# Optimization experiments

Hardware: AMD Instinct MI355X
Metric: run time of the kernel (lower is better)

The kernel has to match this reference:

```python
import jax, jax.numpy as jnp
import numpy as np

N = 25000      # n_nodes
K = 16         # k_sparse (out-degree per node)
E = N * K      # n_edges
D = 12         # depth
U = 48         # units
FEATS = 2
EF = 1
EPS = 1e-5     # BatchNorm eps


def _lin(h, W, b):
    return h @ W.T + b


def _bn(h, g, b):
    # training-mode BatchNorm over dim 0 (biased variance, like torch)
    m = h.mean(0)
    v = jnp.mean((h - m) ** 2, axis=0)
    return (h - m) * jax.lax.rsqrt(v + EPS) * g + b


def setup_inputs():
    key = jax.random.key(0)
    ks = iter(jax.random.split(key, 64))

    def nrm(shape, fan):
        return jax.random.normal(next(ks), shape, dtype=jnp.float32) * float(1.0 / np.sqrt(fan))

    inp = {}
    inp['x'] = jax.random.uniform(next(ks), (N, FEATS), dtype=jnp.float32)
    inp['edge_attr'] = jax.random.uniform(next(ks), (E, EF), dtype=jnp.float32)
    src = jnp.repeat(jnp.arange(N, dtype=jnp.int32), K)            # each node has K out-edges
    dst = jax.random.randint(next(ks), (E,), 0, N, dtype=jnp.int32)
    inp['edge_index'] = jnp.stack([src, dst])                       # [2, E]
    inp['v_lin0_W'] = nrm((U, FEATS), FEATS); inp['v_lin0_b'] = nrm((U,), FEATS)
    for nm in ['vW1', 'vW2', 'vW3', 'vW4']:
        inp[nm] = nrm((D, U, U), U)
    for nm in ['vb1', 'vb2', 'vb3', 'vb4']:
        inp[nm] = nrm((D, U), U)
    inp['vbn_g'] = jnp.ones((D, U), jnp.float32); inp['vbn_b'] = jnp.zeros((D, U), jnp.float32)
    inp['e_lin0_W'] = nrm((U, EF), EF); inp['e_lin0_b'] = nrm((U,), EF)
    inp['eW'] = nrm((D, U, U), U); inp['eb'] = nrm((D, U), U)
    inp['ebn_g'] = jnp.ones((D, U), jnp.float32); inp['ebn_b'] = jnp.zeros((D, U), jnp.float32)
    inp['pW0'] = nrm((U, U), U); inp['pb0'] = nrm((U,), U)
    inp['pW1'] = nrm((U, U), U); inp['pb1'] = nrm((U,), U)
    inp['pW2'] = nrm((1, U), U); inp['pb2'] = nrm((1,), U)
    inp['zW0'] = nrm((U, U), U); inp['zb0'] = nrm((U,), U)
    inp['zW1'] = nrm((1, U), U); inp['zb1'] = nrm((1,), U)
    inp['k_sparse'] = K
    return inp


def _forward(edge_index, k_sparse, x, edge_attr, v_lin0_W, v_lin0_b, vW1, vb1, vW2, vb2, vW3, vb3, vW4, vb4, vbn_g, vbn_b, e_lin0_W, e_lin0_b, eW, eb, ebn_g, ebn_b, pW0, pb0, pW1, pb1, pW2, pb2, zW0, zb0, zW1, zb1):
    n = x.shape[0]
    src, dst = edge_index[0], edge_index[1]
    deg = jnp.maximum(jax.ops.segment_sum(jnp.ones((src.shape[0],), x.dtype), src, num_segments=n), 1.0)
    h = jax.nn.silu(_lin(x, v_lin0_W, v_lin0_b))          # [N, U]
    w = jax.nn.silu(_lin(edge_attr, e_lin0_W, e_lin0_b))  # [E, U]

    def layer(carry, p):
        h, w = carry
        W1, b1, W2, b2, W3, b3, W4, b4, gv, bv, We, be, ge, bee = p
        h1 = _lin(h, W1, b1); h2 = _lin(h, W2, b2)
        h3 = _lin(h, W3, b3); h4 = _lin(h, W4, b4)
        msg = jax.nn.sigmoid(w) * h2[dst]                                 # [E, U] gather + gate
        agg = jax.ops.segment_sum(msg, src, num_segments=n) / deg[:, None]  # scatter-mean to source node
        h_new = h + jax.nn.silu(_bn(h1 + agg, gv, bv))
        w_new = w + jax.nn.silu(_bn(_lin(w, We, be) + h3[src] + h4[dst], ge, bee))
        return (h_new, w_new), None

    (_, w), _ = jax.lax.scan(layer, (h, w), (vW1, vb1, vW2, vb2, vW3, vb3, vW4, vb4, vbn_g, vbn_b, eW, eb, ebn_g, ebn_b))

    # ParNet heuristic head: MLP then group-softmax over k_sparse edges per node
    p = jax.nn.silu(_lin(w, pW0, pb0))
    p = jax.nn.silu(_lin(p, pW1, pb1))
    p = _lin(p, pW2, pb2).reshape(-1, k_sparse)
    heu = jax.nn.softmax(p, axis=1).reshape(-1)                            # [E]
    # Z_net logZ head (mean over edges)
    logZ = jnp.mean(jax.nn.relu(_lin(w, zW0, zb0)) @ zW1.T + zb1, axis=0)  # [1]
    return heu, logZ


def reference(x, edge_attr, edge_index, v_lin0_W, v_lin0_b, vW1, vb1, vW2, vb2, vW3, vb3, vW4, vb4, vbn_g, vbn_b, e_lin0_W, e_lin0_b, eW, eb, ebn_g, ebn_b, pW0, pb0, pW1, pb1, pW2, pb2, zW0, zb0, zW1, zb1, k_sparse):
    return _forward(edge_index, k_sparse, x, edge_attr, v_lin0_W, v_lin0_b, vW1, vb1, vW2, vb2, vW3, vb3, vW4, vb4, vbn_g, vbn_b, e_lin0_W, e_lin0_b, eW, eb, ebn_g, ebn_b, pW0, pb0, pW1, pb1, pW2, pb2, zW0, zb0, zW1, zb1)
```

## Files before the change

### kernel.cpp

```cpp
#include <hip/hip_runtime.h>
#include <hip/hip_bf16.h>
#include <hip/hip_fp16.h>

#define NN 25000
#define KK 16
#define EE 400000
#define DD 12
#define UU 48
#define EPSBN 1e-5f
#define RP 88

using bf16 = __hip_bfloat16;
typedef short bf16x8 __attribute__((ext_vector_type(8)));
typedef short sx8 __attribute__((ext_vector_type(8)));
typedef float f32x4 __attribute__((ext_vector_type(4)));

__device__ __forceinline__ float b2f(bf16 v){ return __bfloat162float(v); }
__device__ __forceinline__ float sigm(float x){ return 1.f/(1.f+__expf(-x)); }
__device__ __forceinline__ float siluf(float x){ return x/(1.f+__expf(-x)); }
__device__ __forceinline__ short f2bs(float f){ bf16 h=__float2bfloat16(f); return *(short*)&h; }
__device__ __forceinline__ float bs2f(short s){ bf16 h; *(short*)&h = s; return __bfloat162float(h); }
__device__ __forceinline__ short f2hs(float f){ __half h=__float2half(f); return *(short*)&h; }
__device__ __forceinline__ float hs2f(short s){ __half h; *(short*)&h = s; return __half2float(h); }

__device__ __forceinline__ float ldx(const void* p, size_t i, bool isb){
  return isb ? b2f(((const bf16*)p)[i]) : ((const float*)p)[i];
}
__device__ __forceinline__ void stout(void* p, size_t i, float v, bool isb){
  if (isb) ((bf16*)p)[i] = __float2bfloat16(v);
  else     ((float*)p)[i] = v;
}
__device__ __forceinline__ bool dflag(const void* vbng){
  return *((const unsigned*)vbng) == 0x3F803F80u;
}
#define LDSFENCE() asm volatile("s_waitcnt lgkmcnt(0)" ::: "memory")

__device__ __forceinline__ void stageW(short* BT, const void* W, size_t WOFF, bool isb, int tid){
  if (isb){
    const short* src = ((const short*)W) + WOFF;
    for (int j=tid; j<288; j+=256){
      int r=j/6, k=(j%6)*8;
      *(bf16x8*)&BT[r*RP+k] = *(const bf16x8*)(src + j*8);
    }
  } else {
    for (int i=tid;i<2304;i+=256){ int r=i/48,k=i%48; BT[r*RP+k]=f2bs(ldx(W,WOFF+i,false)); }
  }
}

__global__ void k_init_nodes(const void* __restrict__ x, const void* __restrict__ W0,
                             const void* __restrict__ b0, float* __restrict__ h,
                             float* __restrict__ stats, float* __restrict__ zpart,
                             const void* __restrict__ fl){
  const bool isb = dflag(fl);
  int gid = blockIdx.x*256 + threadIdx.x;
  if (gid < DD*12288) stats[gid] = 0.f;
  if (gid < 64) zpart[gid] = 0.f;
  if (gid < NN*UU){
    int n = gid/UU, c = gid%UU;
    float acc = ldx(b0,c,isb) + ldx(W0,c*2,isb)*ldx(x,n*2,isb) + ldx(W0,c*2+1,isb)*ldx(x,n*2+1,isb);
    h[gid] = siluf(acc);
  }
}

__global__ void k_init_edges(const void* __restrict__ ea, const void* __restrict__ W0,
                             const void* __restrict__ b0, short* __restrict__ w,
                             const void* __restrict__ fl){
  const bool isb = dflag(fl);
  int gid = blockIdx.x*256 + threadIdx.x;
  if (gid < EE*UU){
    int e = gid/UU, c = gid%UU;
    float acc = ldx(b0,c,isb) + ldx(W0,c,isb)*ldx(ea,e,isb);
    w[gid] = f2hs(siluf(acc));
  }
}

__global__ __launch_bounds__(256) void k_node(
    float* __restrict__ h, float* __restrict__ h1,
    short* __restrict__ h2b, short* __restrict__ h3b, short* __restrict__ h4b,
    const void* __restrict__ W1, const void* __restrict__ W2,
    const void* __restrict__ W3, const void* __restrict__ W4,
    const void* __restrict__ b1, const void* __restrict__ b2,
    const void* __restrict__ b3, const void* __restrict__ b4,
    const void* __restrict__ gv, const void* __restrict__ bv,
    const float* __restrict__ stats, int ctl, const void* __restrict__ fl)
{
  const bool isb = dflag(fl);
  const int d = ctl>>1, apply = ctl&1;
  const size_t WOFF = (size_t)d*UU*UU, BOFF = (size_t)d*UU;
  __shared__ alignas(16) short BT[4][48*RP];
  __shared__ alignas(16) short AT[4][16*RP];
  __shared__ float bL[4][UU];
  __shared__ float scV[96];
  __shared__ float sred[96];
  int tid = threadIdx.x, lane = tid&63, wid = tid>>6;
  const void* Ws[4] = {W1,W2,W3,W4};
  const void* bs[4] = {b1,b2,b3,b4};
  #pragma unroll
  for (int m=0;m<4;m++) stageW(BT[m], Ws[m], WOFF, isb, tid);
  for (int i=tid;i<4*768;i+=256){ int m=i/768, j=i%768; int r=j/16,k=48+(j%16); BT[m][r*RP+k]=0; }
  for (int i=tid;i<4*256;i+=256){ int wv=i/256, j=i%256; int r=j/16,k=48+(j%16); AT[wv][r*RP+k]=0; }
  if (tid<192) bL[tid/48][tid%48] = ldx(bs[tid/48],BOFF+(tid%48),isb);
  if (apply && tid<96){
    const float* sp = stats + (size_t)(d-1)*12288;
    float s=0.f;
    for (int k2=0;k2<64;k2++) s += sp[k2*96+tid];
    sred[tid]=s;
  }
  __syncthreads();
  if (apply && tid<48){
    float mean = sred[tid]/(float)NN;
    float var = sred[48+tid]/(float)NN - mean*mean; if (var<0.f) var=0.f;
    float sc = ldx(gv,(size_t)(d-1)*48+tid,isb) * rsqrtf(var+EPSBN);
    scV[tid]=sc; scV[48+tid]=ldx(bv,(size_t)(d-1)*48+tid,isb) - mean*sc;
  }
  __syncthreads();

  int quad = lane>>4, lrow = lane&15;
  short* A = AT[wid];
  int gw = blockIdx.x*4+wid, gws = gridDim.x*4;
  const int NT = (NN+15)/16;
  for (int t=gw; t<NT; t+=gws){
    int nb = t*16;
    #pragma unroll
    for (int j=0;j<3;j++){
      int f = lane+64*j; int r=f/12, c4=f%12; int n=nb+r;
      short4 s4; s4.x=0;s4.y=0;s4.z=0;s4.w=0;
      if (n<NN){
        size_t gi = (size_t)n*48 + c4*4;
        float4 hv = *(const float4*)&h[gi];
        if (apply){
          float4 yv = *(const float4*)&h1[gi];
          int c0=c4*4;
          hv.x += siluf(scV[c0+0]*yv.x + scV[48+c0+0]);
          hv.y += siluf(scV[c0+1]*yv.y + scV[48+c0+1]);
          hv.z += siluf(scV[c0+2]*yv.z + scV[48+c0+2]);
          hv.w += siluf(scV[c0+3]*yv.w + scV[48+c0+3]);
          *(float4*)&h[gi] = hv;
        }
        s4.x=f2bs(hv.x); s4.y=f2bs(hv.y); s4.z=f2bs(hv.z); s4.w=f2bs(hv.w);
      }
      *(short4*)&A[r*RP + c4*4] = s4;
    }
    LDSFENCE();
    bf16x8 a0 = *(const bf16x8*)&A[lrow*RP + quad*8];
    bf16x8 a1 = *(const bf16x8*)&A[lrow*RP + 32 + quad*8];
    #pragma unroll
    for (int m=0;m<4;m++){
      f32x4 ac0={0,0,0,0}, ac1={0,0,0,0}, ac2={0,0,0,0};
      bf16x8 bfr;
      bfr = *(const bf16x8*)&BT[m][(0+lrow)*RP + quad*8];      ac0=__builtin_amdgcn_mfma_f32_16x16x32_bf16(a0,bfr,ac0,0,0,0);
      bfr = *(const bf16x8*)&BT[m][(0+lrow)*RP + 32 + quad*8]; ac0=__builtin_amdgcn_mfma_f32_16x16x32_bf16(a1,bfr,ac0,0,0,0);
      bfr = *(const bf16x8*)&BT[m][(16+lrow)*RP + quad*8];     ac1=__builtin_amdgcn_mfma_f32_16x16x32_bf16(a0,bfr,ac1,0,0,0);
      bfr = *(const bf16x8*)&BT[m][(16+lrow)*RP + 32 + quad*8];ac1=__builtin_amdgcn_mfma_f32_16x16x32_bf16(a1,bfr,ac1,0,0,0);
      bfr = *(const bf16x8*)&BT[m][(32+lrow)*RP + quad*8];     ac2=__builtin_amdgcn_mfma_f32_16x16x32_bf16(a0,bfr,ac2,0,0,0);
      bfr = *(const bf16x8*)&BT[m][(32+lrow)*RP + 32 + quad*8];ac2=__builtin_amdgcn_mfma_f32_16x16x32_bf16(a1,bfr,ac2,0,0,0);
      #pragma unroll
      for (int nt=0;nt<3;nt++){
        int c = nt*16+lrow;
        f32x4 ac = (nt==0)?ac0:((nt==1)?ac1:ac2);
        float bv2 = bL[m][c];
        #pragma unroll
        for (int r=0;r<4;r++){
          int n = nb + quad*4 + r;
          if (n<NN){
            float v = ac[r] + bv2;
            if (m==0) h1[(size_t)n*48+c] = v;
            else if (m==1) h2b[(size_t)n*48+c] = f2hs(v);
            else if (m==2) h3b[(size_t)n*48+c] = f2hs(v);
            else           h4b[(size_t)n*48+c] = f2hs(v);
          }
        }
      }
    }
  }
}

__global__ __launch_bounds__(256,4) void k_edge(
    short* __restrict__ w, short* __restrict__ tmp,
    float* __restrict__ h1, const short* __restrict__ h2b,
    const short* __restrict__ h3b, const short* __restrict__ h4b,
    const int* __restrict__ dst,
    const void* __restrict__ We, const void* __restrict__ eb,
    const void* __restrict__ ge, const void* __restrict__ be,
    float* __restrict__ stats, int ctl, const void* __restrict__ fl)
{
  const bool isb = dflag(fl);
  const int d = ctl>>1, apply = ctl&1;
  const size_t WOFF = (size_t)d*UU*UU, BOFF = (size_t)d*UU;
  __shared__ alignas(16) short BT[48*RP];
  __shared__ alignas(16) short AT[4][32*RP];
  __shared__ float ebL[UU];
  __shared__ float scE[96];
  __shared__ float sred[96];
  __shared__ float sACC[4][192];
  int tid = threadIdx.x, lane = tid&63, wid = tid>>6;
  stageW(BT, We, WOFF, isb, tid);
  for (int i=tid;i<768;i+=256){ int r=i/16,k=48+(i%16); BT[r*RP+k]=0; }
  for (int i=tid;i<4*512;i+=256){ int wv=i/512, j=i%512; int tile=j/256, jj=j%256;
    int r=jj/16, k=48+(jj%16); AT[wv][tile*16*RP + r*RP + k]=0; }
  if (tid<48) ebL[tid]=ldx(eb,BOFF+tid,isb);
  for (int i=tid;i<768;i+=256) ((float*)sACC)[i]=0.f;
  if (apply && tid<96){
    const float* sp = stats + (size_t)(d-1)*12288 + 6144;
    float s=0.f;
    for (int k2=0;k2<64;k2++) s += sp[k2*96+tid];
    sred[tid]=s;
  }
  __syncthreads();
  if (apply && tid<48){
    float mean = sred[tid]/(float)EE;
    float var = sred[48+tid]/(float)EE - mean*mean; if (var<0.f) var=0.f;
    float sc = ldx(ge,(size_t)(d-1)*48+tid,isb) * rsqrtf(var+EPSBN);
    scE[tid]=sc; scE[48+tid]=ldx(be,(size_t)(d-1)*48+tid,isb) - mean*sc;
  }
  __syncthreads();

  int quad = lane>>4, lrow = lane&15;
  short* A0 = AT[wid];
  short* A1 = AT[wid] + 16*RP;
  float* myStats = stats + (size_t)d*12288;
  float accY[3]={0,0,0}, accY2[3]={0,0,0}, accT[3]={0,0,0}, accT2[3]={0,0,0};
  int gw = blockIdx.x*4+wid, gws = gridDim.x*4;
  const int NP = NN/2;
  for (int p=gw; p<NP; p+=gws){
    int n0 = p*2, n1 = n0+1;
    size_t b0 = (size_t)n0*768, b1 = (size_t)n1*768;
    int4 de0 = *(const int4*)&dst[n0*16 + quad*4];
    int4 de1 = *(const int4*)&dst[n1*16 + quad*4];

    #pragma unroll
    for (int j=0;j<3;j++){
      int idx = lane + 64*j;
      int u = idx/96, jj = idx%96;
      int r = jj/6, c0 = (jj%6)*8;
      size_t bn = u ? b1 : b0;
      short* Au = u ? A1 : A0;
      sx8 w8 = *(const sx8*)&w[bn + r*48 + c0];
      float f[8];
      #pragma unroll
      for (int q=0;q<8;q++) f[q] = hs2f(w8[q]);
      if (apply){
        sx8 t8 = *(const sx8*)&tmp[bn + r*48 + c0];
        #pragma unroll
        for (int q=0;q<8;q++) f[q] += siluf(scE[c0+q]*hs2f(t8[q]) + scE[48+c0+q]);
        sx8 ws8;
        #pragma unroll
        for (int q=0;q<8;q++) ws8[q] = f2hs(f[q]);
        *(sx8*)&w[bn + r*48 + c0] = ws8;
      }
      sx8 a8;
      #pragma unroll
      for (int q=0;q<8;q++) a8[q] = f2bs(f[q]);
      *(sx8*)&Au[r*RP + c0] = a8;
    }
    LDSFENCE();
    bf16x8 a00 = *(const bf16x8*)&A0[lrow*RP + quad*8];
    bf16x8 a01 = *(const bf16x8*)&A0[lrow*RP + 32 + quad*8];
    bf16x8 a10 = *(const bf16x8*)&A1[lrow*RP + quad*8];
    bf16x8 a11 = *(const bf16x8*)&A1[lrow*RP + 32 + quad*8];
    f32x4 acc[2][3];
    #pragma unroll
    for (int u=0;u<2;u++)
      #pragma unroll
      for (int nt=0;nt<3;nt++) acc[u][nt] = (f32x4){0,0,0,0};
    #pragma unroll
    for (int nt=0;nt<3;nt++){
      bf16x8 bf0 = *(const bf16x8*)&BT[(nt*16+lrow)*RP + quad*8];
      bf16x8 bf1 = *(const bf16x8*)&BT[(nt*16+lrow)*RP + 32 + quad*8];
      acc[0][nt]=__builtin_amdgcn_mfma_f32_16x16x32_bf16(a00,bf0,acc[0][nt],0,0,0);
      acc[0][nt]=__builtin_amdgcn_mfma_f32_16x16x32_bf16(a01,bf1,acc[0][nt],0,0,0);
      acc[1][nt]=__builtin_amdgcn_mfma_f32_16x16x32_bf16(a10,bf0,acc[1][nt],0,0,0);
      acc[1][nt]=__builtin_amdgcn_mfma_f32_16x16x32_bf16(a11,bf1,acc[1][nt],0,0,0);
    }
    #pragma unroll
    for (int u=0;u<2;u++){
      int n = n0+u;
      size_t bn = u? b1 : b0;
      short* Au = u? A1 : A0;
      int dei[4];
      if (u==0){ dei[0]=de0.x; dei[1]=de0.y; dei[2]=de0.z; dei[3]=de0.w; }
      else     { dei[0]=de1.x; dei[1]=de1.y; dei[2]=de1.z; dei[3]=de1.w; }
      #pragma unroll
      for (int nt=0;nt<3;nt++){
        int c = nt*16+lrow;
        f32x4 ac = acc[u][nt];
        float bv = ebL[c];
        float h3v = hs2f(h3b[(size_t)n*48+c]);
        float pT=0.f, pT2=0.f, pM=0.f;
        #pragma unroll
        for (int r=0;r<4;r++){
          int e = quad*4+r;
          float t = ac[r] + bv + h3v + hs2f(h4b[(size_t)dei[r]*48+c]);
          tmp[bn + e*48 + c] = f2hs(t);
          pT += t; pT2 += t*t;
          float gate = bs2f(Au[e*RP+c]);
          pM += hs2f(h2b[(size_t)dei[r]*48+c]) * sigm(gate);
        }
        pT  += __shfl_xor(pT,16);  pT  += __shfl_xor(pT,32);
        pT2 += __shfl_xor(pT2,16); pT2 += __shfl_xor(pT2,32);
        pM  += __shfl_xor(pM,16);  pM  += __shfl_xor(pM,32);
        accT[nt] += pT; accT2[nt] += pT2;
        if (u==0){
          if (lane<16){
            float yv = h1[(size_t)n*48+c] + pM*(1.f/16.f);
            h1[(size_t)n*48+c] = yv;
            accY[nt] += yv; accY2[nt] += yv*yv;
          }
        } else {
          if (lane>=16 && lane<32){
            float yv = h1[(size_t)n*48+c] + pM*(1.f/16.f);
            h1[(size_t)n*48+c] = yv;
            accY[nt] += yv; accY2[nt] += yv*yv;
          }
        }
      }
    }
  }
  #pragma unroll
  for (int nt=0;nt<3;nt++){
    accY[nt]  += __shfl_xor(accY[nt],16);
    accY2[nt] += __shfl_xor(accY2[nt],16);
  }
  if (lane<16){
    #pragma unroll
    for (int nt=0;nt<3;nt++){
      int c = nt*16+lane;
      sACC[wid][c]      = accY[nt];
      sACC[wid][48+c]   = accY2[nt];
      sACC[wid][96+c]   = accT[nt];
      sACC[wid][144+c]  = accT2[nt];
    }
  }
  __syncthreads();
  if (tid<192){
    float s = sACC[0][tid]+sACC[1][tid]+sACC[2][tid]+sACC[3][tid];
    int bk = (blockIdx.x&63)*96;
    if (tid<96) atomicAdd(&myStats[bk+tid], s);
    else        atomicAdd(&myStats[6144+bk+(tid-96)], s);
  }
}

__global__ __launch_bounds__(256) void k_head1(
    const short* __restrict__ w, short* __restrict__ tmp,
    const void* __restrict__ pW0, const void* __restrict__ pb0,
    const void* __restrict__ zW0, const void* __restrict__ zb0,
    const void* __restrict__ zW1,
    const void* __restrict__ ge, const void* __restrict__ be,
    const float* __restrict__ stats, float* __restrict__ zpart,
    const void* __restrict__ fl)
{
  const bool isb = dflag(fl);
  __shared__ alignas(16) short BT0[48*RP];
  __shared__ alignas(16) short BT1[48*RP];
  __shared__ alignas(16) short AT[4][16*RP];
  __shared__ float pb0L[UU], zb0L[UU], zW1L[UU];
  __shared__ float scE[96];
  __shared__ float sred[96];
  __shared__ float zS[4];
  int tid = threadIdx.x, lane = tid&63, wid = tid>>6;
  stageW(BT0, pW0, 0, isb, tid);
  stageW(BT1, zW0, 0, isb, tid);
  for (int i=tid;i<768;i+=256){ int r=i/16,k=48+(i%16); BT0[r*RP+k]=0; BT1[r*RP+k]=0; }
  for (int i=tid;i<4*256;i+=256){ int wv=i/256, j=i%256; int r=j/16,k=48+(j%16); AT[wv][r*RP+k]=0; }
  if (tid<48){ pb0L[tid]=ldx(pb0,tid,isb); zb0L[tid]=ldx(zb0,tid,isb); zW1L[tid]=ldx(zW1,tid,isb); }
  if (tid<96){
    const float* sp = stats + (size_t)(DD-1)*12288 + 6144;
    float s=0.f;
    for (int k2=0;k2<64;k2++) s += sp[k2*96+tid];
    sred[tid]=s;
  }
  __syncthreads();
  if (tid<48){
    float mean = sred[tid]/(float)EE;
    float var = sred[48+tid]/(float)EE - mean*mean; if (var<0.f) var=0.f;
    float sc = ldx(ge,(size_t)(DD-1)*48+tid,isb) * rsqrtf(var+EPSBN);
    scE[tid]=sc; scE[48+tid]=ldx(be,(size_t)(DD-1)*48+tid,isb) - mean*sc;
  }
  __syncthreads();

  int quad = lane>>4, lrow = lane&15;
  short* A = AT[wid];
  float zacc = 0.f;
  int gw = blockIdx.x*4+wid, gws = gridDim.x*4;
  for (int n=gw; n<NN; n+=gws){
    size_t basef = (size_t)n*768;
    #pragma unroll
    for (int j=0;j<2;j++){
      int idx = lane + 64*j;
      if (idx < 96){
        int r = idx/6, c0 = (idx%6)*8;
        sx8 w8 = *(const sx8*)&w[basef + r*48 + c0];
        sx8 t8 = *(const sx8*)&tmp[basef + r*48 + c0];
        sx8 a8;
        #pragma unroll
        for (int q=0;q<8;q++){
          float f = hs2f(w8[q]) + siluf(scE[c0+q]*hs2f(t8[q]) + scE[48+c0+q]);
          a8[q] = f2bs(f);
        }
        *(sx8*)&A[r*RP + c0] = a8;
      }
    }
    LDSFENCE();
    bf16x8 a0 = *(const bf16x8*)&A[lrow*RP + quad*8];
    bf16x8 a1 = *(const bf16x8*)&A[lrow*RP + 32 + quad*8];
    f32x4 p0={0,0,0,0}, p1={0,0,0,0}, p2={0,0,0,0};
    f32x4 z0={0,0,0,0}, z1={0,0,0,0}, z2={0,0,0,0};
    bf16x8 bfr;
    bfr=*(const bf16x8*)&BT0[(0+lrow)*RP+quad*8];       p0=__builtin_amdgcn_mfma_f32_16x16x32_bf16(a0,bfr,p0,0,0,0);
    bfr=*(const bf16x8*)&BT0[(0+lrow)*RP+32+quad*8];    p0=__builtin_amdgcn_mfma_f32_16x16x32_bf16(a1,bfr,p0,0,0,0);
    bfr=*(const bf16x8*)&BT0[(16+lrow)*RP+quad*8];      p1=__builtin_amdgcn_mfma_f32_16x16x32_bf16(a0,bfr,p1,0,0,0);
    bfr=*(const bf16x8*)&BT0[(16+lrow)*RP+32+quad*8];   p1=__builtin_amdgcn_mfma_f32_16x16x32_bf16(a1,bfr,p1,0,0,0);
    bfr=*(const bf16x8*)&BT0[(32+lrow)*RP+quad*8];      p2=__builtin_amdgcn_mfma_f32_16x16x32_bf16(a0,bfr,p2,0,0,0);
    bfr=*(const bf16x8*)&BT0[(32+lrow)*RP+32+quad*8];   p2=__builtin_amdgcn_mfma_f32_16x16x32_bf16(a1,bfr,p2,0,0,0);
    bfr=*(const bf16x8*)&BT1[(0+lrow)*RP+quad*8];       z0=__builtin_amdgcn_mfma_f32_16x16x32_bf16(a0,bfr,z0,0,0,0);
    bfr=*(const bf16x8*)&BT1[(0+lrow)*RP+32+quad*8];    z0=__builtin_amdgcn_mfma_f32_16x16x32_bf16(a1,bfr,z0,0,0,0);
    bfr=*(const bf16x8*)&BT1[(16+lrow)*RP+quad*8];      z1=__builtin_amdgcn_mfma_f32_16x16x32_bf16(a0,bfr,z1,0,0,0);
    bfr=*(const bf16x8*)&BT1[(16+lrow)*RP+32+quad*8];   z1=__builtin_amdgcn_mfma_f32_16x16x32_bf16(a1,bfr,z1,0,0,0);
    bfr=*(const bf16x8*)&BT1[(32+lrow)*RP+quad*8];      z2=__builtin_amdgcn_mfma_f32_16x16x32_bf16(a0,bfr,z2,0,0,0);
    bfr=*(const bf16x8*)&BT1[(32+lrow)*RP+32+quad*8];   z2=__builtin_amdgcn_mfma_f32_16x16x32_bf16(a1,bfr,z2,0,0,0);
    #pragma unroll
    for (int nt=0;nt<3;nt++){
      int c = nt*16+lrow;
      f32x4 pp = (nt==0)?p0:((nt==1)?p1:p2);
      f32x4 zz = (nt==0)?z0:((nt==1)?z1:z2);
      float pb = pb0L[c], zb = zb0L[c], zw = zW1L[c];
      #pragma unroll
      for (int r=0;r<4;r++){
        int e = quad*4+r;
        tmp[basef + e*48 + c] = f2bs(siluf(pp[r] + pb));
        float zr = zz[r] + zb;
        zacc += zw * (zr > 0.f ? zr : 0.f);
      }
    }
  }
  zacc += __shfl_xor(zacc,1); zacc += __shfl_xor(zacc,2); zacc += __shfl_xor(zacc,4);
  zacc += __shfl_xor(zacc,8); zacc += __shfl_xor(zacc,16); zacc += __shfl_xor(zacc,32);
  if (lane==0) zS[wid]=zacc;
  __syncthreads();
  if (tid==0) atomicAdd(&zpart[blockIdx.x&63], zS[0]+zS[1]+zS[2]+zS[3]);
}

__global__ __launch_bounds__(256) void k_head2(
    const short* __restrict__ tmp,
    const void* __restrict__ pW1, const void* __restrict__ pb1,
    const void* __restrict__ pW2,
    void* __restrict__ out, const void* __restrict__ fl)
{
  const bool isb = dflag(fl);
  __shared__ alignas(16) short BT[48*RP];
  __shared__ alignas(16) short AT[4][16*RP];
  __shared__ float pb1L[UU], pW2L[UU];
  int tid = threadIdx.x, lane = tid&63, wid = tid>>6;
  stageW(BT, pW1, 0, isb, tid);
  for (int i=tid;i<768;i+=256){ int r=i/16,k=48+(i%16); BT[r*RP+k]=0; }
  for (int i=tid;i<4*256;i+=256){ int wv=i/256, j=i%256; int r=j/16,k=48+(j%16); AT[wv][r*RP+k]=0; }
  if (tid<48){ pb1L[tid]=ldx(pb1,tid,isb); pW2L[tid]=ldx(pW2,tid,isb); }
  __syncthreads();

  int quad = lane>>4, lrow = lane&15;
  short* A = AT[wid];
  int gw = blockIdx.x*4+wid, gws = gridDim.x*4;
  for (int n=gw; n<NN; n+=gws){
    size_t basef = (size_t)n*768;
    #pragma unroll
    for (int j=0;j<2;j++){
      int idx = lane + 64*j;
      if (idx < 96){
        int r = idx/6, c8 = idx%6;
        *(bf16x8*)&A[r*RP + c8*8] = *(const bf16x8*)&tmp[basef + r*48 + c8*8];
      }
    }
    LDSFENCE();
    bf16x8 a0 = *(const bf16x8*)&A[lrow*RP + quad*8];
    bf16x8 a1 = *(const bf16x8*)&A[lrow*RP + 32 + quad*8];
    f32x4 q0={0,0,0,0}, q1={0,0,0,0}, q2={0,0,0,0};
    bf16x8 bfr;
    bfr=*(const bf16x8*)&BT[(0+lrow)*RP+quad*8];       q0=__builtin_amdgcn_mfma_f32_16x16x32_bf16(a0,bfr,q0,0,0,0);
    bfr=*(const bf16x8*)&BT[(0+lrow)*RP+32+quad*8];    q0=__builtin_amdgcn_mfma_f32_16x16x32_bf16(a1,bfr,q0,0,0,0);
    bfr=*(const bf16x8*)&BT[(16+lrow)*RP+quad*8];      q1=__builtin_amdgcn_mfma_f32_16x16x32_bf16(a0,bfr,q1,0,0,0);
    bfr=*(const bf16x8*)&BT[(16+lrow)*RP+32+quad*8];   q1=__builtin_amdgcn_mfma_f32_16x16x32_bf16(a1,bfr,q1,0,0,0);
    bfr=*(const bf16x8*)&BT[(32+lrow)*RP+quad*8];      q2=__builtin_amdgcn_mfma_f32_16x16x32_bf16(a0,bfr,q2,0,0,0);
    bfr=*(const bf16x8*)&BT[(32+lrow)*RP+32+quad*8];   q2=__builtin_amdgcn_mfma_f32_16x16x32_bf16(a1,bfr,q2,0,0,0);
    float pp[4] = {0.f,0.f,0.f,0.f};
    #pragma unroll
    for (int nt=0;nt<3;nt++){
      int c = nt*16+lrow;
      f32x4 qq = (nt==0)?q0:((nt==1)?q1:q2);
      float pb = pb1L[c], pw = pW2L[c];
      #pragma unroll
      for (int r=0;r<4;r++) pp[r] += pw * siluf(qq[r] + pb);
    }
    #pragma unroll
    for (int r=0;r<4;r++){
      pp[r] += __shfl_xor(pp[r],1); pp[r] += __shfl_xor(pp[r],2);
      pp[r] += __shfl_xor(pp[r],4); pp[r] += __shfl_xor(pp[r],8);
    }
    float mx = fmaxf(fmaxf(pp[0],pp[1]), fmaxf(pp[2],pp[3]));
    mx = fmaxf(mx, __shfl_xor(mx,16)); mx = fmaxf(mx, __shfl_xor(mx,32));
    float ex[4]; float se = 0.f;
    #pragma unroll
    for (int r=0;r<4;r++){ ex[r] = __expf(pp[r]-mx); se += ex[r]; }
    se += __shfl_xor(se,16); se += __shfl_xor(se,32);
    float inv = 1.f/se;
    if (lrow==0){
      #pragma unroll
      for (int r=0;r<4;r++) stout(out, (size_t)n*16 + quad*4 + r, ex[r]*inv, isb);
    }
  }
}

__global__ void k_final(const float* __restrict__ zpart, const void* __restrict__ zb1,
                        void* __restrict__ out, const void* __restrict__ fl){
  const bool isb = dflag(fl);
  int tid=threadIdx.x;
  float s = (tid<64) ? zpart[tid] : 0.f;
  s += __shfl_xor(s,1); s += __shfl_xor(s,2); s += __shfl_xor(s,4);
  s += __shfl_xor(s,8); s += __shfl_xor(s,16); s += __shfl_xor(s,32);
  if (tid==0) stout(out, EE, s/(float)EE + ldx(zb1,0,isb), isb);
}

extern "C" void kernel_launch(void* const* d_in, const int* in_sizes, int n_in,
                              void* d_out, int out_size, void* d_ws, size_t ws_size,
                              hipStream_t stream){
  (void)in_sizes; (void)n_in; (void)out_size; (void)ws_size;
  const void* x=d_in[0]; const void* ea=d_in[1];
  const int* ei=(const int*)d_in[2];
  const void* vW0=d_in[3]; const void* vb0=d_in[4];
  const void* vW1=d_in[5]; const void* vW2=d_in[6]; const void* vW3=d_in[7]; const void* vW4=d_in[8];
  const void* vb1=d_in[9]; const void* vb2=d_in[10]; const void* vb3=d_in[11]; const void* vb4=d_in[12];
  const void* vbng=d_in[13]; const void* vbnb=d_in[14];
  const void* eW0=d_in[15]; const void* eb0=d_in[16];
  const void* eW=d_in[17]; const void* ebv=d_in[18];
  const void* ebng=d_in[19]; const void* ebnb=d_in[20];
  const void* pW0=d_in[21]; const void* pb0=d_in[22];
  const void* pW1=d_in[23]; const void* pb1=d_in[24];
  const void* pW2=d_in[25]; const void* pb2=d_in[26]; (void)pb2;
  const void* zW0=d_in[27]; const void* zb0=d_in[28];
  const void* zW1=d_in[29]; const void* zb1=d_in[30];
  const int* dst = ei + EE;
  const void* fl = vbng;

  float* h   = (float*)d_ws;
  float* h1  = h  + (size_t)NN*UU;
  short* h2b = (short*)(h1 + (size_t)NN*UU);
  short* h3b = h2b + (size_t)NN*UU;
  short* h4b = h3b + (size_t)NN*UU;
  short* w   = h4b + (size_t)NN*UU;
  short* tmp = w + (size_t)EE*UU;
  float* stats = (float*)(tmp + (size_t)EE*UU);
  float* zpart = stats + DD*12288;

  k_init_nodes<<<(NN*UU+255)/256,256,0,stream>>>(x,vW0,vb0,h,stats,zpart,fl);
  k_init_edges<<<(EE*UU+255)/256,256,0,stream>>>(ea,eW0,eb0,w,fl);
  for (int d=0; d<DD; d++){
    int ctl = (d<<1) | (d>0 ? 1 : 0);
    k_node<<<512,256,0,stream>>>(h,h1,h2b,h3b,h4b,
        vW1,vW2,vW3,vW4,vb1,vb2,vb3,vb4,vbng,vbnb,stats,ctl,fl);
    k_edge<<<1024,256,0,stream>>>(w,tmp,h1,h2b,h3b,h4b,dst,eW,ebv,ebng,ebnb,stats,ctl,fl);
  }
  k_head1<<<1024,256,0,stream>>>(w,tmp,pW0,pb0,zW0,zb0,zW1,ebng,ebnb,stats,zpart,fl);
  k_head2<<<1024,256,0,stream>>>(tmp,pW1,pb1,pW2,d_out,fl);
  k_final<<<1,64,0,stream>>>(zpart,zb1,d_out,fl);
}
```

Baseline: 1.255 ms.

## Interleave h2/h4 node features for paired gathers and shrink edge LDS padding

```diff
diff --git a/kernel.cpp b/kernel.cpp
--- a/kernel.cpp
+++ b/kernel.cpp
@@ -9,6 +9,7 @@
 #define UU 48
 #define EPSBN 1e-5f
 #define RP 88
+#define RPA 72
 
 using bf16 = __hip_bfloat16;
 typedef short bf16x8 __attribute__((ext_vector_type(8)));
@@ -76,7 +77,7 @@
 
 __global__ __launch_bounds__(256) void k_node(
     float* __restrict__ h, float* __restrict__ h1,
-    short* __restrict__ h2b, short* __restrict__ h3b, short* __restrict__ h4b,
+    short* __restrict__ h24, short* __restrict__ h3b,
     const void* __restrict__ W1, const void* __restrict__ W2,
     const void* __restrict__ W3, const void* __restrict__ W4,
     const void* __restrict__ b1, const void* __restrict__ b2,
@@ -165,9 +166,9 @@
           if (n<NN){
             float v = ac[r] + bv2;
             if (m==0) h1[(size_t)n*48+c] = v;
-            else if (m==1) h2b[(size_t)n*48+c] = f2hs(v);
-            else if (m==2) h3b[(size_t)n*48+c] = f2hs(v);
-            else           h4b[(size_t)n*48+c] = f2hs(v);
+            else if (m==1) h24[(size_t)n*96+c*2]   = f2hs(v);
+            else if (m==2) h3b[(size_t)n*48+c]     = f2hs(v);
+            else           h24[(size_t)n*96+c*2+1] = f2hs(v);
           }
         }
       }
@@ -175,10 +176,10 @@
   }
 }
 
-__global__ __launch_bounds__(256,4) void k_edge(
+__global__ __launch_bounds__(256,5) void k_edge(
     short* __restrict__ w, short* __restrict__ tmp,
-    float* __restrict__ h1, const short* __restrict__ h2b,
-    const short* __restrict__ h3b, const short* __restrict__ h4b,
+    float* __restrict__ h1, const short* __restrict__ h24,
+    const short* __restrict__ h3b,
     const int* __restrict__ dst,
     const void* __restrict__ We, const void* __restrict__ eb,
     const void* __restrict__ ge, const void* __restrict__ be,
@@ -188,7 +189,7 @@
   const int d = ctl>>1, apply = ctl&1;
   const size_t WOFF = (size_t)d*UU*UU, BOFF = (size_t)d*UU;
   __shared__ alignas(16) short BT[48*RP];
-  __shared__ alignas(16) short AT[4][32*RP];
+  __shared__ alignas(16) short AT[4][32*RPA];
   __shared__ float ebL[UU];
   __shared__ float scE[96];
   __shared__ float sred[96];
@@ -197,7 +198,7 @@
   stageW(BT, We, WOFF, isb, tid);
   for (int i=tid;i<768;i+=256){ int r=i/16,k=48+(i%16); BT[r*RP+k]=0; }
   for (int i=tid;i<4*512;i+=256){ int wv=i/512, j=i%512; int tile=j/256, jj=j%256;
-    int r=jj/16, k=48+(jj%16); AT[wv][tile*16*RP + r*RP + k]=0; }
+    int r=jj/16, k=48+(jj%16); AT[wv][tile*16*RPA + r*RPA + k]=0; }
   if (tid<48) ebL[tid]=ldx(eb,BOFF+tid,isb);
   for (int i=tid;i<768;i+=256) ((float*)sACC)[i]=0.f;
   if (apply && tid<96){
@@ -217,7 +218,7 @@
 
   int quad = lane>>4, lrow = lane&15;
   short* A0 = AT[wid];
-  short* A1 = AT[wid] + 16*RP;
+  short* A1 = AT[wid] + 16*RPA;
   float* myStats = stats + (size_t)d*12288;
   float accY[3]={0,0,0}, accY2[3]={0,0,0}, accT[3]={0,0,0}, accT2[3]={0,0,0};
   int gw = blockIdx.x*4+wid, gws = gridDim.x*4;
@@ -251,13 +252,13 @@
       sx8 a8;
       #pragma unroll
       for (int q=0;q<8;q++) a8[q] = f2bs(f[q]);
-      *(sx8*)&Au[r*RP + c0] = a8;
+      *(sx8*)&Au[r*RPA + c0] = a8;
     }
     LDSFENCE();
-    bf16x8 a00 = *(const bf16x8*)&A0[lrow*RP + quad*8];
-    bf16x8 a01 = *(const bf16x8*)&A0[lrow*RP + 32 + quad*8];
-    bf16x8 a10 = *(const bf16x8*)&A1[lrow*RP + quad*8];
-    bf16x8 a11 = *(const bf16x8*)&A1[lrow*RP + 32 + quad*8];
+    bf16x8 a00 = *(const bf16x8*)&A0[lrow*RPA + quad*8];
+    bf16x8 a01 = *(const bf16x8*)&A0[lrow*RPA + 32 + quad*8];
+    bf16x8 a10 = *(const bf16x8*)&A1[lrow*RPA + quad*8];
+    bf16x8 a11 = *(const bf16x8*)&A1[lrow*RPA + 32 + quad*8];
     f32x4 acc[2][3];
     #pragma unroll
     for (int u=0;u<2;u++)
@@ -290,11 +291,15 @@
         #pragma unroll
         for (int r=0;r<4;r++){
           int e = quad*4+r;
-          float t = ac[r] + bv + h3v + hs2f(h4b[(size_t)dei[r]*48+c]);
+          union { unsigned uu; short2 ss; } gpair;
+          gpair.uu = *(const unsigned*)&h24[(size_t)dei[r]*96 + c*2];
+          float h2v = hs2f(gpair.ss.x);
+          float h4v = hs2f(gpair.ss.y);
+          float t = ac[r] + bv + h3v + h4v;
           tmp[bn + e*48 + c] = f2hs(t);
           pT += t; pT2 += t*t;
-          float gate = bs2f(Au[e*RP+c]);
-          pM += hs2f(h2b[(size_t)dei[r]*48+c]) * sigm(gate);
+          float gate = bs2f(Au[e*RPA+c]);
+          pM += h2v * sigm(gate);
         }
         pT  += __shfl_xor(pT,16);  pT  += __shfl_xor(pT,32);
         pT2 += __shfl_xor(pT2,16); pT2 += __shfl_xor(pT2,32);
@@ -542,10 +547,9 @@
 
   float* h   = (float*)d_ws;
   float* h1  = h  + (size_t)NN*UU;
-  short* h2b = (short*)(h1 + (size_t)NN*UU);
-  short* h3b = h2b + (size_t)NN*UU;
-  short* h4b = h3b + (size_t)NN*UU;
-  short* w   = h4b + (size_t)NN*UU;
+  short* h24 = (short*)(h1 + (size_t)NN*UU);
+  short* h3b = h24 + (size_t)NN*96;
+  short* w   = h3b + (size_t)NN*UU;
   short* tmp = w + (size_t)EE*UU;
   float* stats = (float*)(tmp + (size_t)EE*UU);
   float* zpart = stats + DD*12288;
@@ -554,9 +558,9 @@
   k_init_edges<<<(EE*UU+255)/256,256,0,stream>>>(ea,eW0,eb0,w,fl);
   for (int d=0; d<DD; d++){
     int ctl = (d<<1) | (d>0 ? 1 : 0);
-    k_node<<<512,256,0,stream>>>(h,h1,h2b,h3b,h4b,
+    k_node<<<512,256,0,stream>>>(h,h1,h24,h3b,
         vW1,vW2,vW3,vW4,vb1,vb2,vb3,vb4,vbng,vbnb,stats,ctl,fl);
-    k_edge<<<1024,256,0,stream>>>(w,tmp,h1,h2b,h3b,h4b,dst,eW,ebv,ebng,ebnb,stats,ctl,fl);
+    k_edge<<<1280,256,0,stream>>>(w,tmp,h1,h24,h3b,dst,eW,ebv,ebng,ebnb,stats,ctl,fl);
   }
   k_head1<<<1024,256,0,stream>>>(w,tmp,pW0,pb0,zW0,zb0,zW1,ebng,ebnb,stats,zpart,fl);
   k_head2<<<1024,256,0,stream>>>(tmp,pW1,pb1,pW2,d_out,fl);
```

After: 1.542 ms. +22.8%, slower.
